# Optimization experiments

Hardware: AMD Instinct MI355X
Metric: run time of the kernel (lower is better)

## Reference

```python
import jax, jax.numpy as jnp
import numpy as np

B, SQ, SK, D, DV = 2, 1024, 1024, 64, 64
NEG = -1e9


def setup_inputs() -> dict:
    key = jax.random.key(0)
    kq, kk, kv, km = jax.random.split(key, 4)
    return {
        "q": jax.random.normal(kq, (B, SQ, D), dtype=jnp.float32),
        "k": jax.random.normal(kk, (B, SK, D), dtype=jnp.float32),
        "v": jax.random.normal(kv, (B, SK, DV), dtype=jnp.float32),
        "mask": jax.random.randint(km, (B, SK), 0, 2, dtype=jnp.int32),
    }


def reference(q, k, v, mask):
    # L1 (Manhattan) distance scores: [B, Sq, Sk]
    dist = jnp.sum(jnp.abs(q[:, :, None, :] - k[:, None, :, :]), axis=-1)
    scores = -dist
    # mask: [B, Sk] -> broadcast over queries as [B, 1, Sk]
    scores = jnp.where(mask[:, None, :] == 0, NEG, scores)
    attention = jax.nn.softmax(scores, axis=-1)
    # weighted sum of values: [B, Sq, Dv]
    return jnp.einsum("bqk,bkd->bqd", attention, v)
```

## Files before the change

### kernel.cpp

```cpp
#include <hip/hip_runtime.h>
#include <math.h>

#define B_ 2
#define SQ_ 1024
#define SK_ 1024
#define D_ 64
#define DV_ 64
#define QB 4
#define KSPLIT 2
#define KTILE (SK_ / KSPLIT)
#define CE 80.0f
#define QSCALE 2048.0f
#define QINV (1.0f / 2048.0f)


__device__ inline unsigned int pk2(float x, float y) {
  int xi = (int)rintf(fminf(fmaxf(x, -15.9f), 15.9f) * QSCALE) + 32768;
  int yi = (int)rintf(fminf(fmaxf(y, -15.9f), 15.9f) * QSCALE) + 32768;
  return (unsigned int)(xi & 0xffff) | ((unsigned int)yi << 16);
}

__device__ inline unsigned int bfp2(float lo, float hi) {
  union { float f; unsigned int u; } a, b;
  a.f = lo; b.f = hi;
  unsigned int ua = a.u + 0x7fff + ((a.u >> 16) & 1);
  unsigned int ub = b.u + 0x7fff + ((b.u >> 16) & 1);
  return (ua >> 16) | (ub & 0xffff0000u);
}

__global__ __launch_bounds__(256) void convert_qkv(
    const float* __restrict__ qg, const float* __restrict__ kg,
    const float* __restrict__ vg, unsigned int* __restrict__ ws) {
  const int t = blockIdx.x * 256 + threadIdx.x;
  uint4 r;
  if (t < 32768) {
    const float4* s4 = (t < 16384) ? (const float4*)qg : (const float4*)kg;
    const int idx = t & 16383;
    float4 a = s4[idx * 2], b = s4[idx * 2 + 1];
    r.x = pk2(a.x, a.y); r.y = pk2(a.z, a.w);
    r.z = pk2(b.x, b.y); r.w = pk2(b.z, b.w);
  } else {
    const int idx = t - 32768;
    float4 a = ((const float4*)vg)[idx * 2], b = ((const float4*)vg)[idx * 2 + 1];
    r.x = bfp2(a.x, a.y); r.y = bfp2(a.z, a.w);
    r.z = bfp2(b.x, b.y); r.w = bfp2(b.z, b.w);
  }
  ((uint4*)ws)[t] = r;
}

__device__ inline int slot(int kl) { return kl ^ ((kl >> 5) & 3); }

__global__ __launch_bounds__(256, 4) void manh_main(
    const unsigned int* __restrict__ ws, const int* __restrict__ maskg,
    float* __restrict__ ws_o, float* __restrict__ ws_l) {
  __shared__ float4 p4s[KTILE];
  __shared__ float pv[4][QB][DV_];
  __shared__ float4 redl[4];

  const unsigned int* wsq = ws;
  const unsigned int* wsk = ws + 65536;
  const unsigned int* wsv = ws + 131072;

  const int tid = threadIdx.x;
  const int wid = tid >> 6;
  const int split = blockIdx.x & 1;
  const int qgrp = (blockIdx.x >> 1) & 255;
  const int b = blockIdx.x >> 9;
  const int q0 = qgrp * QB;
  const int kbase = split * KTILE;

  const int kq = tid >> 2;
  const int qt = tid & 3;

  const uint4* qrow4 = (const uint4*)(wsq + ((size_t)b * SQ_ + q0) * 32);
  uint4 qr[QB][2];
#pragma unroll
  for (int q = 0; q < QB; ++q) {
    qr[q][0] = qrow4[q * 8 + qt * 2];
    qr[q][1] = qrow4[q * 8 + qt * 2 + 1];
  }

  const uint4* krow4 = (const uint4*)(wsk + (size_t)b * SK_ * 32);
  const int* mb = maskg + (size_t)b * SK_;

  float lsum[QB] = {0.f, 0.f, 0.f, 0.f};
  uint4 kc0 = krow4[(size_t)(kbase + kq) * 8 + qt * 2];
  uint4 kc1 = krow4[(size_t)(kbase + kq) * 8 + qt * 2 + 1];
#pragma unroll 1
  for (int p = 0; p < 8; ++p) {
    const int keyn = kbase + (((p + 1) & 7) << 6) + kq;
    uint4 kn0 = krow4[(size_t)keyn * 8 + qt * 2];
    uint4 kn1 = krow4[(size_t)keyn * 8 + qt * 2 + 1];
    unsigned int d[QB] = {0u, 0u, 0u, 0u};
#pragma unroll
    for (int q = 0; q < QB; ++q) {
      d[q] = __builtin_amdgcn_sad_u16(qr[q][0].x, kc0.x, d[q]);
      d[q] = __builtin_amdgcn_sad_u16(qr[q][0].y, kc0.y, d[q]);
      d[q] = __builtin_amdgcn_sad_u16(qr[q][0].z, kc0.z, d[q]);
      d[q] = __builtin_amdgcn_sad_u16(qr[q][0].w, kc0.w, d[q]);
      d[q] = __builtin_amdgcn_sad_u16(qr[q][1].x, kc1.x, d[q]);
      d[q] = __builtin_amdgcn_sad_u16(qr[q][1].y, kc1.y, d[q]);
      d[q] = __builtin_amdgcn_sad_u16(qr[q][1].z, kc1.z, d[q]);
      d[q] = __builtin_amdgcn_sad_u16(qr[q][1].w, kc1.w, d[q]);
    }
#pragma unroll
    for (int q = 0; q < QB; ++q) {
      d[q] += __shfl_xor(d[q], 1, 64);
      d[q] += __shfl_xor(d[q], 2, 64);
    }
    if ((tid & 3) == (p & 3)) {
      const int kl = (p << 6) + kq;
      const int mk = mb[kbase + kl];
      float4 e;
      e.x = mk ? __expf(fmaf(-(float)d[0], QINV, CE)) : 0.f;
      e.y = mk ? __expf(fmaf(-(float)d[1], QINV, CE)) : 0.f;
      e.z = mk ? __expf(fmaf(-(float)d[2], QINV, CE)) : 0.f;
      e.w = mk ? __expf(fmaf(-(float)d[3], QINV, CE)) : 0.f;
      p4s[slot(kl)] = e;
      lsum[0] += e.x; lsum[1] += e.y; lsum[2] += e.z; lsum[3] += e.w;
    }
    kc0 = kn0; kc1 = kn1;
  }
#pragma unroll
  for (int off = 32; off > 0; off >>= 1)
#pragma unroll
    for (int q = 0; q < QB; ++q) lsum[q] += __shfl_down(lsum[q], off, 64);
  if ((tid & 63) == 0)
    redl[wid] = make_float4(lsum[0], lsum[1], lsum[2], lsum[3]);
  __syncthreads();

  const int col = tid & 15;
  const int chunk = tid >> 4;
  const uint2* vb2 = (const uint2*)(wsv + (size_t)b * SK_ * 32);
  float4 acc[QB];
#pragma unroll
  for (int q = 0; q < QB; ++q) acc[q] = make_float4(0.f, 0.f, 0.f, 0.f);
#pragma unroll 8
  for (int t = 0; t < 32; ++t) {
    const int kl = chunk * 32 + t;
    uint2 vr = vb2[(size_t)(kbase + kl) * 16 + col];
    float4 pw = p4s[slot(kl)];
    union { unsigned int u; float f; } v0, v1, v2, v3;
    v0.u = vr.x << 16; v1.u = vr.x & 0xffff0000u;
    v2.u = vr.y << 16; v3.u = vr.y & 0xffff0000u;
    acc[0].x += pw.x * v0.f; acc[0].y += pw.x * v1.f;
    acc[0].z += pw.x * v2.f; acc[0].w += pw.x * v3.f;
    acc[1].x += pw.y * v0.f; acc[1].y += pw.y * v1.f;
    acc[1].z += pw.y * v2.f; acc[1].w += pw.y * v3.f;
    acc[2].x += pw.z * v0.f; acc[2].y += pw.z * v1.f;
    acc[2].z += pw.z * v2.f; acc[2].w += pw.z * v3.f;
    acc[3].x += pw.w * v0.f; acc[3].y += pw.w * v1.f;
    acc[3].z += pw.w * v2.f; acc[3].w += pw.w * v3.f;
  }
#pragma unroll
  for (int q = 0; q < QB; ++q) {
    acc[q].x += __shfl_xor(acc[q].x, 16, 64);
    acc[q].y += __shfl_xor(acc[q].y, 16, 64);
    acc[q].z += __shfl_xor(acc[q].z, 16, 64);
    acc[q].w += __shfl_xor(acc[q].w, 16, 64);
    acc[q].x += __shfl_xor(acc[q].x, 32, 64);
    acc[q].y += __shfl_xor(acc[q].y, 32, 64);
    acc[q].z += __shfl_xor(acc[q].z, 32, 64);
    acc[q].w += __shfl_xor(acc[q].w, 32, 64);
  }
  if ((tid & 63) < 16) {
#pragma unroll
    for (int q = 0; q < QB; ++q) ((float4*)&pv[wid][q][0])[col] = acc[q];
  }
  __syncthreads();

  const int q2 = tid >> 6;
  const int d2 = tid & 63;
  float o = pv[0][q2][d2] + pv[1][q2][d2] + pv[2][q2][d2] + pv[3][q2][d2];
  const size_t row = (size_t)b * SQ_ + q0 + q2;
  ws_o[(row * KSPLIT + split) * DV_ + d2] = o;
  if (d2 == 0) {
    float l = redl[0].x * 0.f;
    const float* rl = (const float*)redl;
    l = rl[0 * 4 + q2] + rl[1 * 4 + q2] + rl[2 * 4 + q2] + rl[3 * 4 + q2];
    ws_l[row * KSPLIT + split] = l;
  }
}

__global__ __launch_bounds__(256) void manh_combine(
    const float* __restrict__ ws_o, const float* __restrict__ ws_l,
    float* __restrict__ outg) {
  const int gid = blockIdx.x * 256 + threadIdx.x;
  const int r = gid >> 6;
  const int d = gid & 63;
  const float l = ws_l[r * 2] + ws_l[r * 2 + 1];
  const float o = ws_o[(r * 2) * DV_ + d] + ws_o[(r * 2 + 1) * DV_ + d];
  outg[(size_t)r * DV_ + d] = o / l;
}

extern "C" void kernel_launch(void* const* d_in, const int* in_sizes, int n_in,
                              void* d_out, int out_size, void* d_ws,
                              size_t ws_size, hipStream_t stream) {
  const float* q = (const float*)d_in[0];
  const float* k = (const float*)d_in[1];
  const float* v = (const float*)d_in[2];
  const int* mask = (const int*)d_in[3];
  float* out = (float*)d_out;

  unsigned int* ws = (unsigned int*)d_ws;
  float* ws_o = (float*)(ws + 196608);
  float* ws_l = (float*)(ws + 458752);

  convert_qkv<<<dim3(192), dim3(256), 0, stream>>>(q, k, v, ws);
  manh_main<<<dim3(B_ * (SQ_ / QB) * KSPLIT), dim3(256), 0, stream>>>(
      ws, mask, ws_o, ws_l);
  manh_combine<<<dim3(B_ * SQ_ * DV_ / 256), dim3(256), 0, stream>>>(
      ws_o, ws_l, out);
}
```

Before: 75.95 us.

## Stage K and V tiles through double-buffered LDS with four-way key split

The key range is split into four tiles instead of two, which doubles the grid. Each block cooperatively copies its K tile and then its V tile into a double-buffered shared-memory staging area, loading the next chunk into registers while computing on the current one. The SAD score and PV passes then read from LDS instead of issuing per-thread global loads, and the staging buffer is reused for the final per-wave reduction. In exchange, LDS use grows to about 36KB per block, which may limit occupancy, the combine kernel now reads four partials, and the exp offset constant is lowered.

```diff
diff --git a/kernel.cpp b/kernel.cpp
--- a/kernel.cpp
+++ b/kernel.cpp
@@ -7,9 +7,9 @@
 #define D_ 64
 #define DV_ 64
 #define QB 4
-#define KSPLIT 2
-#define KTILE (SK_ / KSPLIT)
-#define CE 80.0f
+#define KSPLIT 4
+#define KTILE 256
+#define CE 60.0f
 #define QSCALE 2048.0f
 #define QINV (1.0f / 2048.0f)
 
@@ -48,13 +48,11 @@
   ((uint4*)ws)[t] = r;
 }
 
-__device__ inline int slot(int kl) { return kl ^ ((kl >> 5) & 3); }
-
 __global__ __launch_bounds__(256, 4) void manh_main(
     const unsigned int* __restrict__ ws, const int* __restrict__ maskg,
     float* __restrict__ ws_o, float* __restrict__ ws_l) {
+  __shared__ uint4 stage[2][1024];
   __shared__ float4 p4s[KTILE];
-  __shared__ float pv[4][QB][DV_];
   __shared__ float4 redl[4];
 
   const unsigned int* wsq = ws;
@@ -63,9 +61,9 @@
 
   const int tid = threadIdx.x;
   const int wid = tid >> 6;
-  const int split = blockIdx.x & 1;
-  const int qgrp = (blockIdx.x >> 1) & 255;
-  const int b = blockIdx.x >> 9;
+  const int split = blockIdx.x & 3;
+  const int qgrp = (blockIdx.x >> 2) & 255;
+  const int b = blockIdx.x >> 10;
   const int q0 = qgrp * QB;
   const int kbase = split * KTILE;
 
@@ -80,17 +78,29 @@
     qr[q][1] = qrow4[q * 8 + qt * 2 + 1];
   }
 
-  const uint4* krow4 = (const uint4*)(wsk + (size_t)b * SK_ * 32);
-  const int* mb = maskg + (size_t)b * SK_;
+  const uint4* ksrc = (const uint4*)(wsk + (size_t)b * SK_ * 32) + kbase * 8;
+  const uint4* vsrc = (const uint4*)(wsv + (size_t)b * SK_ * 32) + kbase * 8;
+  const int* mb = maskg + (size_t)b * SK_ + kbase;
+
+  uint4 r0, r1, r2, r3;
+#define LOADC(src, c)                                   \
+  r0 = (src)[(c) * 1024 + tid];                         \
+  r1 = (src)[(c) * 1024 + tid + 256];                   \
+  r2 = (src)[(c) * 1024 + tid + 512];                   \
+  r3 = (src)[(c) * 1024 + tid + 768];
+#define WRITEC(buf)                                     \
+  stage[buf][tid] = r0;                                 \
+  stage[buf][tid + 256] = r1;                           \
+  stage[buf][tid + 512] = r2;                           \
+  stage[buf][tid + 768] = r3;
 
   float lsum[QB] = {0.f, 0.f, 0.f, 0.f};
-  uint4 kc0 = krow4[(size_t)(kbase + kq) * 8 + qt * 2];
-  uint4 kc1 = krow4[(size_t)(kbase + kq) * 8 + qt * 2 + 1];
-#pragma unroll 1
-  for (int p = 0; p < 8; ++p) {
-    const int keyn = kbase + (((p + 1) & 7) << 6) + kq;
-    uint4 kn0 = krow4[(size_t)keyn * 8 + qt * 2];
-    uint4 kn1 = krow4[(size_t)keyn * 8 + qt * 2 + 1];
+
+  auto sad_pass = [&](int buf, int p) {
+    const int kl = (p & 1) * 64 + kq;
+    const uint4* kb = &stage[buf][0];
+    uint4 kc0 = kb[kl * 8 + qt * 2];
+    uint4 kc1 = kb[kl * 8 + qt * 2 + 1];
     unsigned int d[QB] = {0u, 0u, 0u, 0u};
 #pragma unroll
     for (int q = 0; q < QB; ++q) {
@@ -108,50 +118,63 @@
       d[q] += __shfl_xor(d[q], 1, 64);
       d[q] += __shfl_xor(d[q], 2, 64);
     }
-    if ((tid & 3) == (p & 3)) {
-      const int kl = (p << 6) + kq;
-      const int mk = mb[kbase + kl];
+    if ((tid & 3) == p) {
+      const int key = p * 64 + kq;
+      const int mk = mb[key];
       float4 e;
       e.x = mk ? __expf(fmaf(-(float)d[0], QINV, CE)) : 0.f;
       e.y = mk ? __expf(fmaf(-(float)d[1], QINV, CE)) : 0.f;
       e.z = mk ? __expf(fmaf(-(float)d[2], QINV, CE)) : 0.f;
       e.w = mk ? __expf(fmaf(-(float)d[3], QINV, CE)) : 0.f;
-      p4s[slot(kl)] = e;
+      p4s[key] = e;
       lsum[0] += e.x; lsum[1] += e.y; lsum[2] += e.z; lsum[3] += e.w;
     }
-    kc0 = kn0; kc1 = kn1;
-  }
+  };
+
+  const int col = tid & 15;
+  const int slot = (tid >> 4) & 15;
+  float4 acc[QB];
+#pragma unroll
+  for (int q = 0; q < QB; ++q) acc[q] = make_float4(0.f, 0.f, 0.f, 0.f);
+
+  auto pv_chunk = [&](int buf, int vi) {
+#pragma unroll
+    for (int t = 0; t < 8; ++t) {
+      const int kl = slot + 16 * t;
+      uint2 vr = ((const uint2*)&stage[buf][0])[kl * 16 + col];
+      float4 pw = p4s[vi * 128 + kl];
+      union { unsigned int u; float f; } v0, v1, v2, v3;
+      v0.u = vr.x << 16; v1.u = vr.x & 0xffff0000u;
+      v2.u = vr.y << 16; v3.u = vr.y & 0xffff0000u;
+      acc[0].x += pw.x * v0.f; acc[0].y += pw.x * v1.f;
+      acc[0].z += pw.x * v2.f; acc[0].w += pw.x * v3.f;
+      acc[1].x += pw.y * v0.f; acc[1].y += pw.y * v1.f;
+      acc[1].z += pw.y * v2.f; acc[1].w += pw.y * v3.f;
+      acc[2].x += pw.z * v0.f; acc[2].y += pw.z * v1.f;
+      acc[2].z += pw.z * v2.f; acc[2].w += pw.z * v3.f;
+      acc[3].x += pw.w * v0.f; acc[3].y += pw.w * v1.f;
+      acc[3].z += pw.w * v2.f; acc[3].w += pw.w * v3.f;
+    }
+  };
+
+  LOADC(ksrc, 0); WRITEC(0); __syncthreads();
+  LOADC(ksrc, 1);
+  sad_pass(0, 0); sad_pass(0, 1);
+  WRITEC(1); __syncthreads();
+  LOADC(vsrc, 0);
+  sad_pass(1, 2); sad_pass(1, 3);
 #pragma unroll
   for (int off = 32; off > 0; off >>= 1)
 #pragma unroll
     for (int q = 0; q < QB; ++q) lsum[q] += __shfl_down(lsum[q], off, 64);
   if ((tid & 63) == 0)
     redl[wid] = make_float4(lsum[0], lsum[1], lsum[2], lsum[3]);
-  __syncthreads();
-
-  const int col = tid & 15;
-  const int chunk = tid >> 4;
-  const uint2* vb2 = (const uint2*)(wsv + (size_t)b * SK_ * 32);
-  float4 acc[QB];
-#pragma unroll
-  for (int q = 0; q < QB; ++q) acc[q] = make_float4(0.f, 0.f, 0.f, 0.f);
-#pragma unroll 8
-  for (int t = 0; t < 32; ++t) {
-    const int kl = chunk * 32 + t;
-    uint2 vr = vb2[(size_t)(kbase + kl) * 16 + col];
-    float4 pw = p4s[slot(kl)];
-    union { unsigned int u; float f; } v0, v1, v2, v3;
-    v0.u = vr.x << 16; v1.u = vr.x & 0xffff0000u;
-    v2.u = vr.y << 16; v3.u = vr.y & 0xffff0000u;
-    acc[0].x += pw.x * v0.f; acc[0].y += pw.x * v1.f;
-    acc[0].z += pw.x * v2.f; acc[0].w += pw.x * v3.f;
-    acc[1].x += pw.y * v0.f; acc[1].y += pw.y * v1.f;
-    acc[1].z += pw.y * v2.f; acc[1].w += pw.y * v3.f;
-    acc[2].x += pw.z * v0.f; acc[2].y += pw.z * v1.f;
-    acc[2].z += pw.z * v2.f; acc[2].w += pw.z * v3.f;
-    acc[3].x += pw.w * v0.f; acc[3].y += pw.w * v1.f;
-    acc[3].z += pw.w * v2.f; acc[3].w += pw.w * v3.f;
-  }
+  WRITEC(0); __syncthreads();
+  LOADC(vsrc, 1);
+  pv_chunk(0, 0);
+  WRITEC(1); __syncthreads();
+  pv_chunk(1, 1);
+
 #pragma unroll
   for (int q = 0; q < QB; ++q) {
     acc[q].x += __shfl_xor(acc[q].x, 16, 64);
@@ -163,23 +186,28 @@
     acc[q].z += __shfl_xor(acc[q].z, 32, 64);
     acc[q].w += __shfl_xor(acc[q].w, 32, 64);
   }
+  __syncthreads();
+  float* pvf = (float*)&stage[0][0];
   if ((tid & 63) < 16) {
 #pragma unroll
-    for (int q = 0; q < QB; ++q) ((float4*)&pv[wid][q][0])[col] = acc[q];
+    for (int q = 0; q < QB; ++q)
+      ((float4*)&pvf[(wid * QB + q) * DV_])[col] = acc[q];
   }
   __syncthreads();
 
   const int q2 = tid >> 6;
   const int d2 = tid & 63;
-  float o = pv[0][q2][d2] + pv[1][q2][d2] + pv[2][q2][d2] + pv[3][q2][d2];
+  float o = pvf[(0 * QB + q2) * DV_ + d2] + pvf[(1 * QB + q2) * DV_ + d2] +
+            pvf[(2 * QB + q2) * DV_ + d2] + pvf[(3 * QB + q2) * DV_ + d2];
   const size_t row = (size_t)b * SQ_ + q0 + q2;
   ws_o[(row * KSPLIT + split) * DV_ + d2] = o;
   if (d2 == 0) {
-    float l = redl[0].x * 0.f;
     const float* rl = (const float*)redl;
-    l = rl[0 * 4 + q2] + rl[1 * 4 + q2] + rl[2 * 4 + q2] + rl[3 * 4 + q2];
+    float l = rl[0 * 4 + q2] + rl[1 * 4 + q2] + rl[2 * 4 + q2] + rl[3 * 4 + q2];
     ws_l[row * KSPLIT + split] = l;
   }
+#undef LOADC
+#undef WRITEC
 }
 
 __global__ __launch_bounds__(256) void manh_combine(
@@ -188,8 +216,10 @@
   const int gid = blockIdx.x * 256 + threadIdx.x;
   const int r = gid >> 6;
   const int d = gid & 63;
-  const float l = ws_l[r * 2] + ws_l[r * 2 + 1];
-  const float o = ws_o[(r * 2) * DV_ + d] + ws_o[(r * 2 + 1) * DV_ + d];
+  const float l = ws_l[r * 4] + ws_l[r * 4 + 1] + ws_l[r * 4 + 2] +
+                  ws_l[r * 4 + 3];
+  const float o = ws_o[(r * 4 + 0) * DV_ + d] + ws_o[(r * 4 + 1) * DV_ + d] +
+                  ws_o[(r * 4 + 2) * DV_ + d] + ws_o[(r * 4 + 3) * DV_ + d];
   outg[(size_t)r * DV_ + d] = o / l;
 }
 
@@ -204,7 +234,7 @@
 
   unsigned int* ws = (unsigned int*)d_ws;
   float* ws_o = (float*)(ws + 196608);
-  float* ws_l = (float*)(ws + 458752);
+  float* ws_l = (float*)(ws + 720896);
 
   convert_qkv<<<dim3(192), dim3(256), 0, stream>>>(q, k, v, ws);
   manh_main<<<dim3(B_ * (SQ_ / QB) * KSPLIT), dim3(256), 0, stream>>>(
```

New measurement: 80.22 us. 5.6% more time.

## Split keys eight ways with one key per thread and smaller blocks

Applied to the files above, without the earlier changes.

Raises the key split from 2 to 8 and shrinks blocks to 128 threads, each thread owning a full key row, so no cross-lane shuffle reduction is needed for distances. Query rows are staged once in shared memory and the P·V stage is reorganised so each thread accumulates two output columns over 32 keys. The combine kernel now sums eight partials, which enlarges the workspace partials and the combine traffic. The exponent offset constant is lowered to keep the partial sums in range.

```diff
diff --git a/kernel.cpp b/kernel.cpp
--- a/kernel.cpp
+++ b/kernel.cpp
@@ -7,9 +7,10 @@
 #define D_ 64
 #define DV_ 64
 #define QB 4
-#define KSPLIT 2
-#define KTILE (SK_ / KSPLIT)
-#define CE 80.0f
+#define KSPLIT 8
+#define KTILE 128
+#define TPB 128
+#define CE 60.0f
 #define QSCALE 2048.0f
 #define QINV (1.0f / 2048.0f)
 
@@ -48,137 +49,97 @@
   ((uint4*)ws)[t] = r;
 }
 
-__device__ inline int slot(int kl) { return kl ^ ((kl >> 5) & 3); }
-
-__global__ __launch_bounds__(256, 4) void manh_main(
+__global__ __launch_bounds__(TPB, 8) void manh_main(
     const unsigned int* __restrict__ ws, const int* __restrict__ maskg,
     float* __restrict__ ws_o, float* __restrict__ ws_l) {
+  __shared__ uint4 qs[QB * 8];
   __shared__ float4 p4s[KTILE];
-  __shared__ float pv[4][QB][DV_];
-  __shared__ float4 redl[4];
+  __shared__ float pvf[4][QB][DV_];
+  __shared__ float4 redl[2];
 
   const unsigned int* wsq = ws;
   const unsigned int* wsk = ws + 65536;
   const unsigned int* wsv = ws + 131072;
 
   const int tid = threadIdx.x;
-  const int wid = tid >> 6;
-  const int split = blockIdx.x & 1;
-  const int qgrp = (blockIdx.x >> 1) & 255;
-  const int b = blockIdx.x >> 9;
+  const int split = blockIdx.x & 7;
+  const int qgrp = (blockIdx.x >> 3) & 255;
+  const int b = blockIdx.x >> 11;
   const int q0 = qgrp * QB;
   const int kbase = split * KTILE;
 
-  const int kq = tid >> 2;
-  const int qt = tid & 3;
+  if (tid < 32)
+    qs[tid] = ((const uint4*)(wsq + ((size_t)b * SQ_ + q0) * 32))[tid];
+  __syncthreads();
 
-  const uint4* qrow4 = (const uint4*)(wsq + ((size_t)b * SQ_ + q0) * 32);
-  uint4 qr[QB][2];
-#pragma unroll
-  for (int q = 0; q < QB; ++q) {
-    qr[q][0] = qrow4[q * 8 + qt * 2];
-    qr[q][1] = qrow4[q * 8 + qt * 2 + 1];
-  }
-
-  const uint4* krow4 = (const uint4*)(wsk + (size_t)b * SK_ * 32);
-  const int* mb = maskg + (size_t)b * SK_;
-
-  float lsum[QB] = {0.f, 0.f, 0.f, 0.f};
-  uint4 kc0 = krow4[(size_t)(kbase + kq) * 8 + qt * 2];
-  uint4 kc1 = krow4[(size_t)(kbase + kq) * 8 + qt * 2 + 1];
-#pragma unroll 1
-  for (int p = 0; p < 8; ++p) {
-    const int keyn = kbase + (((p + 1) & 7) << 6) + kq;
-    uint4 kn0 = krow4[(size_t)keyn * 8 + qt * 2];
-    uint4 kn1 = krow4[(size_t)keyn * 8 + qt * 2 + 1];
-    unsigned int d[QB] = {0u, 0u, 0u, 0u};
+  const int key = kbase + tid;
+  const uint4* kr = (const uint4*)(wsk + (size_t)b * SK_ * 32) + (size_t)key * 8;
+  unsigned int d[QB] = {0u, 0u, 0u, 0u};
+#pragma unroll 2
+  for (int j = 0; j < 8; ++j) {
+    const uint4 kc = kr[j];
 #pragma unroll
     for (int q = 0; q < QB; ++q) {
-      d[q] = __builtin_amdgcn_sad_u16(qr[q][0].x, kc0.x, d[q]);
-      d[q] = __builtin_amdgcn_sad_u16(qr[q][0].y, kc0.y, d[q]);
-      d[q] = __builtin_amdgcn_sad_u16(qr[q][0].z, kc0.z, d[q]);
-      d[q] = __builtin_amdgcn_sad_u16(qr[q][0].w, kc0.w, d[q]);
-      d[q] = __builtin_amdgcn_sad_u16(qr[q][1].x, kc1.x, d[q]);
-      d[q] = __builtin_amdgcn_sad_u16(qr[q][1].y, kc1.y, d[q]);
-      d[q] = __builtin_amdgcn_sad_u16(qr[q][1].z, kc1.z, d[q]);
-      d[q] = __builtin_amdgcn_sad_u16(qr[q][1].w, kc1.w, d[q]);
+      const uint4 qv = qs[q * 8 + j];
+      d[q] = __builtin_amdgcn_sad_u16(qv.x, kc.x, d[q]);
+      d[q] = __builtin_amdgcn_sad_u16(qv.y, kc.y, d[q]);
+      d[q] = __builtin_amdgcn_sad_u16(qv.z, kc.z, d[q]);
+      d[q] = __builtin_amdgcn_sad_u16(qv.w, kc.w, d[q]);
     }
-#pragma unroll
-    for (int q = 0; q < QB; ++q) {
-      d[q] += __shfl_xor(d[q], 1, 64);
-      d[q] += __shfl_xor(d[q], 2, 64);
-    }
-    if ((tid & 3) == (p & 3)) {
-      const int kl = (p << 6) + kq;
-      const int mk = mb[kbase + kl];
-      float4 e;
-      e.x = mk ? __expf(fmaf(-(float)d[0], QINV, CE)) : 0.f;
-      e.y = mk ? __expf(fmaf(-(float)d[1], QINV, CE)) : 0.f;
-      e.z = mk ? __expf(fmaf(-(float)d[2], QINV, CE)) : 0.f;
-      e.w = mk ? __expf(fmaf(-(float)d[3], QINV, CE)) : 0.f;
-      p4s[slot(kl)] = e;
-      lsum[0] += e.x; lsum[1] += e.y; lsum[2] += e.z; lsum[3] += e.w;
-    }
-    kc0 = kn0; kc1 = kn1;
   }
+  const int mk = maskg[(size_t)b * SK_ + key];
+  float4 e;
+  e.x = mk ? __expf(fmaf(-(float)d[0], QINV, CE)) : 0.f;
+  e.y = mk ? __expf(fmaf(-(float)d[1], QINV, CE)) : 0.f;
+  e.z = mk ? __expf(fmaf(-(float)d[2], QINV, CE)) : 0.f;
+  e.w = mk ? __expf(fmaf(-(float)d[3], QINV, CE)) : 0.f;
+  p4s[tid] = e;
+
+  float lsum[QB] = {e.x, e.y, e.z, e.w};
 #pragma unroll
   for (int off = 32; off > 0; off >>= 1)
 #pragma unroll
     for (int q = 0; q < QB; ++q) lsum[q] += __shfl_down(lsum[q], off, 64);
   if ((tid & 63) == 0)
-    redl[wid] = make_float4(lsum[0], lsum[1], lsum[2], lsum[3]);
+    redl[tid >> 6] = make_float4(lsum[0], lsum[1], lsum[2], lsum[3]);
   __syncthreads();
 
-  const int col = tid & 15;
-  const int chunk = tid >> 4;
-  const uint2* vb2 = (const uint2*)(wsv + (size_t)b * SK_ * 32);
-  float4 acc[QB];
-#pragma unroll
-  for (int q = 0; q < QB; ++q) acc[q] = make_float4(0.f, 0.f, 0.f, 0.f);
-#pragma unroll 8
+  const int kg = tid >> 5;
+  const int c = tid & 31;
+  const unsigned int* vb = wsv + (size_t)b * SK_ * 32 +
+                           (size_t)(kbase + kg * 32) * 32 + c;
+  float a0x = 0.f, a0y = 0.f, a1x = 0.f, a1y = 0.f;
+  float a2x = 0.f, a2y = 0.f, a3x = 0.f, a3y = 0.f;
+#pragma unroll 4
   for (int t = 0; t < 32; ++t) {
-    const int kl = chunk * 32 + t;
-    uint2 vr = vb2[(size_t)(kbase + kl) * 16 + col];
-    float4 pw = p4s[slot(kl)];
-    union { unsigned int u; float f; } v0, v1, v2, v3;
-    v0.u = vr.x << 16; v1.u = vr.x & 0xffff0000u;
-    v2.u = vr.y << 16; v3.u = vr.y & 0xffff0000u;
-    acc[0].x += pw.x * v0.f; acc[0].y += pw.x * v1.f;
-    acc[0].z += pw.x * v2.f; acc[0].w += pw.x * v3.f;
-    acc[1].x += pw.y * v0.f; acc[1].y += pw.y * v1.f;
-    acc[1].z += pw.y * v2.f; acc[1].w += pw.y * v3.f;
-    acc[2].x += pw.z * v0.f; acc[2].y += pw.z * v1.f;
-    acc[2].z += pw.z * v2.f; acc[2].w += pw.z * v3.f;
-    acc[3].x += pw.w * v0.f; acc[3].y += pw.w * v1.f;
-    acc[3].z += pw.w * v2.f; acc[3].w += pw.w * v3.f;
+    const unsigned int vr = vb[(size_t)t * 32];
+    const float4 pw = p4s[kg * 32 + t];
+    union { unsigned int u; float f; } v0, v1;
+    v0.u = vr << 16; v1.u = vr & 0xffff0000u;
+    a0x += pw.x * v0.f; a0y += pw.x * v1.f;
+    a1x += pw.y * v0.f; a1y += pw.y * v1.f;
+    a2x += pw.z * v0.f; a2y += pw.z * v1.f;
+    a3x += pw.w * v0.f; a3y += pw.w * v1.f;
   }
-#pragma unroll
-  for (int q = 0; q < QB; ++q) {
-    acc[q].x += __shfl_xor(acc[q].x, 16, 64);
-    acc[q].y += __shfl_xor(acc[q].y, 16, 64);
-    acc[q].z += __shfl_xor(acc[q].z, 16, 64);
-    acc[q].w += __shfl_xor(acc[q].w, 16, 64);
-    acc[q].x += __shfl_xor(acc[q].x, 32, 64);
-    acc[q].y += __shfl_xor(acc[q].y, 32, 64);
-    acc[q].z += __shfl_xor(acc[q].z, 32, 64);
-    acc[q].w += __shfl_xor(acc[q].w, 32, 64);
-  }
-  if ((tid & 63) < 16) {
-#pragma unroll
-    for (int q = 0; q < QB; ++q) ((float4*)&pv[wid][q][0])[col] = acc[q];
-  }
+  *(float2*)&pvf[kg][0][c * 2] = make_float2(a0x, a0y);
+  *(float2*)&pvf[kg][1][c * 2] = make_float2(a1x, a1y);
+  *(float2*)&pvf[kg][2][c * 2] = make_float2(a2x, a2y);
+  *(float2*)&pvf[kg][3][c * 2] = make_float2(a3x, a3y);
   __syncthreads();
 
-  const int q2 = tid >> 6;
-  const int d2 = tid & 63;
-  float o = pv[0][q2][d2] + pv[1][q2][d2] + pv[2][q2][d2] + pv[3][q2][d2];
-  const size_t row = (size_t)b * SQ_ + q0 + q2;
-  ws_o[(row * KSPLIT + split) * DV_ + d2] = o;
-  if (d2 == 0) {
-    float l = redl[0].x * 0.f;
-    const float* rl = (const float*)redl;
-    l = rl[0 * 4 + q2] + rl[1 * 4 + q2] + rl[2 * 4 + q2] + rl[3 * 4 + q2];
-    ws_l[row * KSPLIT + split] = l;
+#pragma unroll
+  for (int r = 0; r < 2; ++r) {
+    const int idx = tid + r * TPB;
+    const int q2 = idx >> 6;
+    const int d2 = idx & 63;
+    const float o = pvf[0][q2][d2] + pvf[1][q2][d2] + pvf[2][q2][d2] +
+                    pvf[3][q2][d2];
+    const size_t row = (size_t)b * SQ_ + q0 + q2;
+    ws_o[(row * KSPLIT + split) * DV_ + d2] = o;
+    if (d2 == 0) {
+      const float* rl = (const float*)redl;
+      ws_l[row * KSPLIT + split] = rl[q2] + rl[4 + q2];
+    }
   }
 }
 
@@ -188,8 +149,12 @@
   const int gid = blockIdx.x * 256 + threadIdx.x;
   const int r = gid >> 6;
   const int d = gid & 63;
-  const float l = ws_l[r * 2] + ws_l[r * 2 + 1];
-  const float o = ws_o[(r * 2) * DV_ + d] + ws_o[(r * 2 + 1) * DV_ + d];
+  float l = 0.f, o = 0.f;
+#pragma unroll
+  for (int s = 0; s < KSPLIT; ++s) {
+    l += ws_l[r * KSPLIT + s];
+    o += ws_o[(r * KSPLIT + s) * DV_ + d];
+  }
   outg[(size_t)r * DV_ + d] = o / l;
 }
 
@@ -204,10 +169,10 @@
 
   unsigned int* ws = (unsigned int*)d_ws;
   float* ws_o = (float*)(ws + 196608);
-  float* ws_l = (float*)(ws + 458752);
+  float* ws_l = (float*)(ws + 1245184);
 
   convert_qkv<<<dim3(192), dim3(256), 0, stream>>>(q, k, v, ws);
-  manh_main<<<dim3(B_ * (SQ_ / QB) * KSPLIT), dim3(256), 0, stream>>>(
+  manh_main<<<dim3(B_ * (SQ_ / QB) * KSPLIT), dim3(TPB), 0, stream>>>(
       ws, mask, ws_o, ws_l);
   manh_combine<<<dim3(B_ * SQ_ * DV_ / 256), dim3(256), 0, stream>>>(
       ws_o, ws_l, out);
```

Result: no change. 76.98 us (+1.4%).

## Double query block to 8 rows and split keys four ways

Applied to the files above, without the earlier changes.

Raises the queries per block from 4 to 8 so each loaded key and value row is reused across twice as many queries, and raises the key split from 2 to 4, keeping the grid at 1024 blocks. Query rows are staged through shared memory, the software-prefetched key loop becomes a fully unrolled 4-step loop, and the exp offset constant changes from 80 to 60. This cuts redundant K/V global traffic per query at the cost of more registers for accumulators and more partial outputs for the combine kernel to reduce.

```diff
diff --git a/kernel.cpp b/kernel.cpp
--- a/kernel.cpp
+++ b/kernel.cpp
@@ -6,10 +6,11 @@
 #define SK_ 1024
 #define D_ 64
 #define DV_ 64
-#define QB 4
-#define KSPLIT 2
-#define KTILE (SK_ / KSPLIT)
-#define CE 80.0f
+#define QB 8
+#define KSPLIT 4
+#define KTILE 256
+#define TPB 256
+#define CE 60.0f
 #define QSCALE 2048.0f
 #define QINV (1.0f / 2048.0f)
 
@@ -27,6 +28,8 @@
   unsigned int ub = b.u + 0x7fff + ((b.u >> 16) & 1);
   return (ua >> 16) | (ub & 0xffff0000u);
 }
+
+__device__ inline int slot(int key) { return key ^ ((key >> 4) & 3); }
 
 __global__ __launch_bounds__(256) void convert_qkv(
     const float* __restrict__ qg, const float* __restrict__ kg,
@@ -48,14 +51,13 @@
   ((uint4*)ws)[t] = r;
 }
 
-__device__ inline int slot(int kl) { return kl ^ ((kl >> 5) & 3); }
-
-__global__ __launch_bounds__(256, 4) void manh_main(
+__global__ __launch_bounds__(TPB, 4) void manh_main(
     const unsigned int* __restrict__ ws, const int* __restrict__ maskg,
     float* __restrict__ ws_o, float* __restrict__ ws_l) {
-  __shared__ float4 p4s[KTILE];
-  __shared__ float pv[4][QB][DV_];
-  __shared__ float4 redl[4];
+  __shared__ unsigned int qs_u[QB * 32];
+  __shared__ float4 p4s[2][KTILE];
+  __shared__ float pvf[4][QB][DV_];
+  __shared__ float redl[4][QB];
 
   const unsigned int* wsq = ws;
   const unsigned int* wsk = ws + 65536;
@@ -63,35 +65,36 @@
 
   const int tid = threadIdx.x;
   const int wid = tid >> 6;
-  const int split = blockIdx.x & 1;
-  const int qgrp = (blockIdx.x >> 1) & 255;
+  const int split = blockIdx.x & 3;
+  const int qgrp = (blockIdx.x >> 2) & 127;
   const int b = blockIdx.x >> 9;
   const int q0 = qgrp * QB;
   const int kbase = split * KTILE;
 
+  qs_u[tid] = wsq[((size_t)b * SQ_ + q0) * 32 + tid];
+  __syncthreads();
+
   const int kq = tid >> 2;
   const int qt = tid & 3;
 
-  const uint4* qrow4 = (const uint4*)(wsq + ((size_t)b * SQ_ + q0) * 32);
   uint4 qr[QB][2];
 #pragma unroll
   for (int q = 0; q < QB; ++q) {
-    qr[q][0] = qrow4[q * 8 + qt * 2];
-    qr[q][1] = qrow4[q * 8 + qt * 2 + 1];
-  }
-
-  const uint4* krow4 = (const uint4*)(wsk + (size_t)b * SK_ * 32);
-  const int* mb = maskg + (size_t)b * SK_;
-
-  float lsum[QB] = {0.f, 0.f, 0.f, 0.f};
-  uint4 kc0 = krow4[(size_t)(kbase + kq) * 8 + qt * 2];
-  uint4 kc1 = krow4[(size_t)(kbase + kq) * 8 + qt * 2 + 1];
-#pragma unroll 1
-  for (int p = 0; p < 8; ++p) {
-    const int keyn = kbase + (((p + 1) & 7) << 6) + kq;
-    uint4 kn0 = krow4[(size_t)keyn * 8 + qt * 2];
-    uint4 kn1 = krow4[(size_t)keyn * 8 + qt * 2 + 1];
-    unsigned int d[QB] = {0u, 0u, 0u, 0u};
+    qr[q][0] = *(const uint4*)&qs_u[q * 32 + qt * 8];
+    qr[q][1] = *(const uint4*)&qs_u[q * 32 + qt * 8 + 4];
+  }
+
+  const uint4* krow = (const uint4*)(wsk + (size_t)b * SK_ * 32);
+  const int* mb = maskg + (size_t)b * SK_ + kbase;
+
+  float lsum[QB] = {0.f, 0.f, 0.f, 0.f, 0.f, 0.f, 0.f, 0.f};
+#pragma unroll
+  for (int p = 0; p < 4; ++p) {
+    const int kl = p * 64 + kq;
+    const uint4* kr = krow + (size_t)(kbase + kl) * 8 + qt * 2;
+    const uint4 kc0 = kr[0];
+    const uint4 kc1 = kr[1];
+    unsigned int d[QB] = {0u, 0u, 0u, 0u, 0u, 0u, 0u, 0u};
 #pragma unroll
     for (int q = 0; q < QB; ++q) {
       d[q] = __builtin_amdgcn_sad_u16(qr[q][0].x, kc0.x, d[q]);
@@ -108,25 +111,32 @@
       d[q] += __shfl_xor(d[q], 1, 64);
       d[q] += __shfl_xor(d[q], 2, 64);
     }
-    if ((tid & 3) == (p & 3)) {
-      const int kl = (p << 6) + kq;
-      const int mk = mb[kbase + kl];
-      float4 e;
-      e.x = mk ? __expf(fmaf(-(float)d[0], QINV, CE)) : 0.f;
-      e.y = mk ? __expf(fmaf(-(float)d[1], QINV, CE)) : 0.f;
-      e.z = mk ? __expf(fmaf(-(float)d[2], QINV, CE)) : 0.f;
-      e.w = mk ? __expf(fmaf(-(float)d[3], QINV, CE)) : 0.f;
-      p4s[slot(kl)] = e;
-      lsum[0] += e.x; lsum[1] += e.y; lsum[2] += e.z; lsum[3] += e.w;
-    }
-    kc0 = kn0; kc1 = kn1;
-  }
+    if (qt == p) {
+      const int mk = mb[kl];
+      float4 ea, eb;
+      ea.x = mk ? __expf(fmaf(-(float)d[0], QINV, CE)) : 0.f;
+      ea.y = mk ? __expf(fmaf(-(float)d[1], QINV, CE)) : 0.f;
+      ea.z = mk ? __expf(fmaf(-(float)d[2], QINV, CE)) : 0.f;
+      ea.w = mk ? __expf(fmaf(-(float)d[3], QINV, CE)) : 0.f;
+      eb.x = mk ? __expf(fmaf(-(float)d[4], QINV, CE)) : 0.f;
+      eb.y = mk ? __expf(fmaf(-(float)d[5], QINV, CE)) : 0.f;
+      eb.z = mk ? __expf(fmaf(-(float)d[6], QINV, CE)) : 0.f;
+      eb.w = mk ? __expf(fmaf(-(float)d[7], QINV, CE)) : 0.f;
+      p4s[0][slot(kl)] = ea;
+      p4s[1][slot(kl)] = eb;
+      lsum[0] += ea.x; lsum[1] += ea.y; lsum[2] += ea.z; lsum[3] += ea.w;
+      lsum[4] += eb.x; lsum[5] += eb.y; lsum[6] += eb.z; lsum[7] += eb.w;
+    }
+  }
+
 #pragma unroll
   for (int off = 32; off > 0; off >>= 1)
 #pragma unroll
     for (int q = 0; q < QB; ++q) lsum[q] += __shfl_down(lsum[q], off, 64);
-  if ((tid & 63) == 0)
-    redl[wid] = make_float4(lsum[0], lsum[1], lsum[2], lsum[3]);
+  if ((tid & 63) == 0) {
+#pragma unroll
+    for (int q = 0; q < QB; ++q) redl[wid][q] = lsum[q];
+  }
   __syncthreads();
 
   const int col = tid & 15;
@@ -135,22 +145,31 @@
   float4 acc[QB];
 #pragma unroll
   for (int q = 0; q < QB; ++q) acc[q] = make_float4(0.f, 0.f, 0.f, 0.f);
-#pragma unroll 8
-  for (int t = 0; t < 32; ++t) {
-    const int kl = chunk * 32 + t;
-    uint2 vr = vb2[(size_t)(kbase + kl) * 16 + col];
-    float4 pw = p4s[slot(kl)];
+#pragma unroll 4
+  for (int t = 0; t < 16; ++t) {
+    const int kl = chunk * 16 + t;
+    const uint2 vr = vb2[(size_t)(kbase + kl) * 16 + col];
+    const float4 pa = p4s[0][slot(kl)];
+    const float4 pb = p4s[1][slot(kl)];
     union { unsigned int u; float f; } v0, v1, v2, v3;
     v0.u = vr.x << 16; v1.u = vr.x & 0xffff0000u;
     v2.u = vr.y << 16; v3.u = vr.y & 0xffff0000u;
-    acc[0].x += pw.x * v0.f; acc[0].y += pw.x * v1.f;
-    acc[0].z += pw.x * v2.f; acc[0].w += pw.x * v3.f;
-    acc[1].x += pw.y * v0.f; acc[1].y += pw.y * v1.f;
-    acc[1].z += pw.y * v2.f; acc[1].w += pw.y * v3.f;
-    acc[2].x += pw.z * v0.f; acc[2].y += pw.z * v1.f;
-    acc[2].z += pw.z * v2.f; acc[2].w += pw.z * v3.f;
-    acc[3].x += pw.w * v0.f; acc[3].y += pw.w * v1.f;
-    acc[3].z += pw.w * v2.f; acc[3].w += pw.w * v3.f;
+    acc[0].x += pa.x * v0.f; acc[0].y += pa.x * v1.f;
+    acc[0].z += pa.x * v2.f; acc[0].w += pa.x * v3.f;
+    acc[1].x += pa.y * v0.f; acc[1].y += pa.y * v1.f;
+    acc[1].z += pa.y * v2.f; acc[1].w += pa.y * v3.f;
+    acc[2].x += pa.z * v0.f; acc[2].y += pa.z * v1.f;
+    acc[2].z += pa.z * v2.f; acc[2].w += pa.z * v3.f;
+    acc[3].x += pa.w * v0.f; acc[3].y += pa.w * v1.f;
+    acc[3].z += pa.w * v2.f; acc[3].w += pa.w * v3.f;
+    acc[4].x += pb.x * v0.f; acc[4].y += pb.x * v1.f;
+    acc[4].z += pb.x * v2.f; acc[4].w += pb.x * v3.f;
+    acc[5].x += pb.y * v0.f; acc[5].y += pb.y * v1.f;
+    acc[5].z += pb.y * v2.f; acc[5].w += pb.y * v3.f;
+    acc[6].x += pb.z * v0.f; acc[6].y += pb.z * v1.f;
+    acc[6].z += pb.z * v2.f; acc[6].w += pb.z * v3.f;
+    acc[7].x += pb.w * v0.f; acc[7].y += pb.w * v1.f;
+    acc[7].z += pb.w * v2.f; acc[7].w += pb.w * v3.f;
   }
 #pragma unroll
   for (int q = 0; q < QB; ++q) {
@@ -165,20 +184,23 @@
   }
   if ((tid & 63) < 16) {
 #pragma unroll
-    for (int q = 0; q < QB; ++q) ((float4*)&pv[wid][q][0])[col] = acc[q];
+    for (int q = 0; q < QB; ++q) ((float4*)&pvf[wid][q][0])[col] = acc[q];
   }
   __syncthreads();
 
-  const int q2 = tid >> 6;
-  const int d2 = tid & 63;
-  float o = pv[0][q2][d2] + pv[1][q2][d2] + pv[2][q2][d2] + pv[3][q2][d2];
-  const size_t row = (size_t)b * SQ_ + q0 + q2;
-  ws_o[(row * KSPLIT + split) * DV_ + d2] = o;
-  if (d2 == 0) {
-    float l = redl[0].x * 0.f;
-    const float* rl = (const float*)redl;
-    l = rl[0 * 4 + q2] + rl[1 * 4 + q2] + rl[2 * 4 + q2] + rl[3 * 4 + q2];
-    ws_l[row * KSPLIT + split] = l;
+#pragma unroll
+  for (int r = 0; r < 2; ++r) {
+    const int idx = tid + r * TPB;
+    const int q2 = idx >> 6;
+    const int d2 = idx & 63;
+    const float o = pvf[0][q2][d2] + pvf[1][q2][d2] + pvf[2][q2][d2] +
+                    pvf[3][q2][d2];
+    const size_t row = (size_t)b * SQ_ + q0 + q2;
+    ws_o[(row * KSPLIT + split) * DV_ + d2] = o;
+    if (d2 == 0) {
+      ws_l[row * KSPLIT + split] =
+          redl[0][q2] + redl[1][q2] + redl[2][q2] + redl[3][q2];
+    }
   }
 }
 
@@ -188,8 +210,12 @@
   const int gid = blockIdx.x * 256 + threadIdx.x;
   const int r = gid >> 6;
   const int d = gid & 63;
-  const float l = ws_l[r * 2] + ws_l[r * 2 + 1];
-  const float o = ws_o[(r * 2) * DV_ + d] + ws_o[(r * 2 + 1) * DV_ + d];
+  float l = 0.f, o = 0.f;
+#pragma unroll
+  for (int s = 0; s < KSPLIT; ++s) {
+    l += ws_l[r * KSPLIT + s];
+    o += ws_o[(r * KSPLIT + s) * DV_ + d];
+  }
   outg[(size_t)r * DV_ + d] = o / l;
 }
 
@@ -204,10 +230,10 @@
 
   unsigned int* ws = (unsigned int*)d_ws;
   float* ws_o = (float*)(ws + 196608);
-  float* ws_l = (float*)(ws + 458752);
+  float* ws_l = (float*)(ws + 720896);
 
   convert_qkv<<<dim3(192), dim3(256), 0, stream>>>(q, k, v, ws);
-  manh_main<<<dim3(B_ * (SQ_ / QB) * KSPLIT), dim3(256), 0, stream>>>(
+  manh_main<<<dim3(B_ * (SQ_ / QB) * KSPLIT), dim3(TPB), 0, stream>>>(
       ws, mask, ws_o, ws_l);
   manh_combine<<<dim3(B_ * SQ_ * DV_ / 256), dim3(256), 0, stream>>>(
       ws_o, ws_l, out);
```

Measured after the change: 77.28 us. About the same (+1.7%).
